# Kernel optimization log

Measured on AMD Instinct MI355X. Metric: run time of the kernel, lower is better.

The kernel has to match this reference:

```python
import jax, jax.numpy as jnp
import numpy as np

B, C, H, W, HEADS = 8, 256, 64, 64, 4
EPS = 1e-5  # torch InstanceNorm2d default eps


def conv1x1(x, w):
    # w: [out_c, in_c]; x: [b, in_c, h, w]
    return jnp.einsum('oc,bchw->bohw', w, x)


def maxpool2(x):
    b, c, h, w = x.shape
    return x.reshape(b, c, h // 2, 2, w // 2, 2).max(axis=(3, 5))


def inorm_affine(x, g, b):
    # InstanceNorm2d(affine=True): normalize per (batch, channel) over H,W
    m = jnp.mean(x, axis=(2, 3), keepdims=True)
    v = jnp.mean((x - m) ** 2, axis=(2, 3), keepdims=True)
    return (x - m) * jax.lax.rsqrt(v + EPS) * g[None, :, None, None] + b[None, :, None, None]


def setup_inputs() -> dict:
    key = jax.random.key(0)
    ks = jax.random.split(key, 12)
    s = 1.0 / np.sqrt(C)  # fan-in style scaling for 1x1 conv weights
    return {
        'x': jax.random.normal(ks[0], (B, C, H, W), jnp.float32),
        'theta_w': jax.random.normal(ks[1], (C, C), jnp.float32) * s,
        'phi_w': jax.random.normal(ks[2], (C, C), jnp.float32) * s,
        'g_w': jax.random.normal(ks[3], (C // 2, C), jnp.float32) * s,
        'o_w': jax.random.normal(ks[4], (C, C // 2), jnp.float32) * np.sqrt(2.0 / C),
        'nt_w': 1.0 + 0.1 * jax.random.normal(ks[5], (C,), jnp.float32),
        'nt_b': 0.1 * jax.random.normal(ks[6], (C,), jnp.float32),
        'np_w': 1.0 + 0.1 * jax.random.normal(ks[7], (C,), jnp.float32),
        'np_b': 0.1 * jax.random.normal(ks[8], (C,), jnp.float32),
        'ng_w': 1.0 + 0.1 * jax.random.normal(ks[9], (C // 2,), jnp.float32),
        'ng_b': 0.1 * jax.random.normal(ks[10], (C // 2,), jnp.float32),
        'gamma': jnp.float32(0.5),
    }


def reference(x, theta_w, phi_w, g_w, o_w, nt_w, nt_b, np_w, np_b, ng_w, ng_b, gamma):
    b, c, h, w = x.shape
    n = h * w            # query length
    m = n // 4           # key/value length after 2x2 maxpool
    theta = inorm_affine(conv1x1(x, theta_w), nt_w, nt_b)
    phi = inorm_affine(maxpool2(conv1x1(x, phi_w)), np_w, np_b)
    g = inorm_affine(maxpool2(conv1x1(x, g_w)), ng_w, ng_b)
    # custom head layout: channel dim split as (C//heads, heads), head dim INNER
    theta_ = theta.reshape(b, c // HEADS, HEADS, n)
    phi_ = phi.reshape(b, c // HEADS, HEADS, m)
    g_ = g.reshape(b, (c // 2) // HEADS, HEADS, m)
    beta = jax.nn.softmax(jnp.einsum('bchi,bchj->bhij', theta_, phi_), axis=-1)
    o = jnp.einsum('bchj,bhij->bchi', g_, beta).reshape(b, c // 2, h, w)
    o = conv1x1(o, o_w)
    return gamma * o + x
```

## Files before the change

### kernel.cpp

```cpp
#include <hip/hip_runtime.h>
#include <hip/hip_bf16.h>
#include <math.h>

typedef float f32x4 __attribute__((ext_vector_type(4)));
typedef float f32x16 __attribute__((ext_vector_type(16)));
typedef __bf16 b16x8 __attribute__((ext_vector_type(8)));
typedef __bf16 b16x4 __attribute__((ext_vector_type(4)));
typedef unsigned int u32x2 __attribute__((ext_vector_type(2)));
typedef unsigned int u32x4 __attribute__((ext_vector_type(4)));

#define L2E 1.44269504088896340736f

__global__ void prep_weights(const float* tw, const float* pw, const float* gw,
                             const float* ow, __bf16* Wp, __bf16* OWp) {
    int idx = blockIdx.x * 256 + threadIdx.x;
    if (idx < 640 * 256) {
        int m = idx >> 8, k = idx & 255;
        float v;
        if (m < 256)      { int o = ((m & 63) << 2) + (m >> 6);            v = tw[o * 256 + k]; }
        else if (m < 512) { int mm = m - 256; int o = ((mm & 63) << 2) + (mm >> 6); v = pw[o * 256 + k]; }
        else              { int mm = m - 512; int o = ((mm & 31) << 2) + (mm >> 5); v = gw[o * 256 + k]; }
        Wp[idx] = (__bf16)v;
    } else {
        int j = idx - 640 * 256;
        if (j < 256 * 128) {
            int m = j >> 7, c = j & 127;
            int o = ((c & 31) << 2) + (c >> 5);
            OWp[j] = (__bf16)ow[m * 128 + o];
        }
    }
}

__global__ void transpose_x(const float* x, __bf16* xt) {
    __shared__ float tile[32][33];
    int b = blockIdx.z, c0 = blockIdx.y * 32, p0 = blockIdx.x * 32;
    int tx = threadIdx.x & 31, ty = threadIdx.x >> 5;
#pragma unroll
    for (int i = 0; i < 4; i++) {
        int cy = ty + i * 8;
        tile[cy][tx] = x[((size_t)(b * 256 + c0 + cy)) * 4096 + p0 + tx];
    }
    __syncthreads();
#pragma unroll
    for (int i = 0; i < 4; i++) {
        int py = ty + i * 8;
        xt[((size_t)b * 4096 + p0 + py) * 256 + c0 + tx] = (__bf16)tile[tx][py];
    }
}

__global__ __launch_bounds__(256) void conv_gemm(const __bf16* __restrict__ Wp,
                                                 const __bf16* __restrict__ xt,
                                                 __bf16* theta_t, __bf16* phi_t, __bf16* g_t) {
    int b = blockIdx.z, mt = blockIdx.y, nt = blockIdx.x;
    __shared__ __bf16 Al[128 * 40];
    __shared__ __bf16 Bl[128 * 40];
    int tid = threadIdx.x, l = tid & 63, w = tid >> 6;
    int wm = w >> 1, wn = w & 1, lr = l & 15, lg = l >> 4;
    f32x4 acc[4][4];
#pragma unroll
    for (int i = 0; i < 4; i++)
#pragma unroll
        for (int j = 0; j < 4; j++)
#pragma unroll
            for (int r = 0; r < 4; r++) acc[i][j][r] = 0.f;
    const __bf16* Ag = Wp + (size_t)mt * 128 * 256;
    const __bf16* Bg = xt + ((size_t)b * 4096 + nt * 128) * 256;
    int srow = tid >> 2, scol = (tid & 3) * 8;
    for (int k0 = 0; k0 < 256; k0 += 32) {
        __syncthreads();
#pragma unroll
        for (int hh = 0; hh < 2; hh++) {
            int r = srow + hh * 64;
            *(b16x8*)&Al[r * 40 + scol] = *(const b16x8*)&Ag[(size_t)r * 256 + k0 + scol];
            *(b16x8*)&Bl[r * 40 + scol] = *(const b16x8*)&Bg[(size_t)r * 256 + k0 + scol];
        }
        __syncthreads();
        int ko = lg * 8;
        b16x8 af[4], bfr[4];
#pragma unroll
        for (int i = 0; i < 4; i++) af[i]  = *(b16x8*)&Al[(wm * 64 + i * 16 + lr) * 40 + ko];
#pragma unroll
        for (int i = 0; i < 4; i++) bfr[i] = *(b16x8*)&Bl[(wn * 64 + i * 16 + lr) * 40 + ko];
#pragma unroll
        for (int i = 0; i < 4; i++)
#pragma unroll
            for (int j = 0; j < 4; j++)
                acc[i][j] = __builtin_amdgcn_mfma_f32_16x16x32_bf16(af[i], bfr[j], acc[i][j], 0, 0, 0);
    }
    int rbase = lg * 4;
#pragma unroll
    for (int i = 0; i < 4; i++) {
        int m = mt * 128 + wm * 64 + i * 16 + rbase;
#pragma unroll
        for (int j = 0; j < 4; j++) {
            int p = nt * 128 + wn * 64 + j * 16 + lr;
            b16x4 v;
#pragma unroll
            for (int r = 0; r < 4; r++) v[r] = (__bf16)acc[i][j][r];
            if (m < 256)      *(b16x4*)&theta_t[((size_t)b * 4096 + p) * 256 + m] = v;
            else if (m < 512) *(b16x4*)&phi_t[((size_t)b * 4096 + p) * 256 + (m - 256)] = v;
            else              *(b16x4*)&g_t[((size_t)b * 4096 + p) * 128 + (m - 512)] = v;
        }
    }
}

__global__ void theta_stats(const __bf16* __restrict__ src, float* p1, float* p2) {
    int b = blockIdx.y, rc = blockIdx.x, c = threadIdx.x;
    float a1 = 0.f, a2 = 0.f;
    for (int r = 0; r < 256; r++) {
        float v = (float)src[((size_t)b * 4096 + rc * 256 + r) * 256 + c];
        a1 += v; a2 += v * v;
    }
    p1[(b * 16 + rc) * 256 + c] = a1;
    p2[(b * 16 + rc) * 256 + c] = a2;
}

__global__ void pool_phi(const __bf16* __restrict__ src, __bf16* dst, float* p1, float* p2) {
    int b = blockIdx.y, qc = blockIdx.x, c = threadIdx.x;
    float a1 = 0.f, a2 = 0.f;
    for (int qq = 0; qq < 32; qq++) {
        int q = qc * 32 + qq, qy = q >> 5, qx = q & 31;
        size_t base = ((size_t)(b * 4096) + qy * 128 + qx * 2) * 256 + c;
        float v0 = (float)src[base], v1 = (float)src[base + 256];
        float v2 = (float)src[base + 16384], v3 = (float)src[base + 16640];
        float m = fmaxf(fmaxf(v0, v1), fmaxf(v2, v3));
        dst[((size_t)b * 1024 + q) * 256 + c] = (__bf16)m;
        a1 += m; a2 += m * m;
    }
    p1[(b * 32 + qc) * 256 + c] = a1;
    p2[(b * 32 + qc) * 256 + c] = a2;
}

__global__ __launch_bounds__(256) void pool_gT(const __bf16* __restrict__ src, __bf16* gT,
                                               float* p1, float* p2) {
    __shared__ __bf16 Pt[64][136];
    int b = blockIdx.y, qc = blockIdx.x;
    int t = threadIdx.x, c = t & 127, qh = t >> 7;
    float a1 = 0.f, a2 = 0.f;
    for (int qq = 0; qq < 32; qq++) {
        int ql = qh * 32 + qq, q = qc * 64 + ql;
        int qy = q >> 5, qx = q & 31;
        size_t base = ((size_t)(b * 4096) + qy * 128 + qx * 2) * 128 + c;
        float v0 = (float)src[base], v1 = (float)src[base + 128];
        float v2 = (float)src[base + 8192], v3 = (float)src[base + 8320];
        float m = fmaxf(fmaxf(v0, v1), fmaxf(v2, v3));
        Pt[ql][c] = (__bf16)m;
        a1 += m; a2 += m * m;
    }
    p1[(b * 16 + qc) * 256 + t] = a1;
    p2[(b * 16 + qc) * 256 + t] = a2;
    __syncthreads();
    int hh = c >> 5, ch = c & 31;
#pragma unroll
    for (int sg = 0; sg < 4; sg++) {
        int seg = qh * 4 + sg;
        b16x8 v;
#pragma unroll
        for (int e = 0; e < 8; e++) v[e] = Pt[seg * 8 + e][c];
        *(b16x8*)&gT[((((size_t)(b * 4 + hh) * 16 + qc) * 8 + seg) * 32 + ch) * 8] = v;
    }
}

__global__ void finalize_stats(const float* tp1, const float* tp2, const float* pp1,
                               const float* pp2, const float* gp1, const float* gp2,
                               const float* ntw, const float* ntb, const float* npw,
                               const float* npb, const float* ngw, const float* ngb,
                               float* sct, float* bit, float* scp, float* bip,
                               float* scg, float* big) {
    int idx = blockIdx.x * 256 + threadIdx.x;
    if (idx >= 8 * 640) return;
    int b = idx / 640, c = idx % 640;
    if (c < 256) {
        float s1 = 0.f, s2 = 0.f;
        for (int i = 0; i < 16; i++) { s1 += tp1[(b * 16 + i) * 256 + c]; s2 += tp2[(b * 16 + i) * 256 + c]; }
        float n = 4096.f;
        float m = s1 / n, v = s2 / n - m * m;
        float r = rsqrtf(v + 1e-5f);
        int o = ((c & 63) << 2) + (c >> 6);
        float wv = ntw[o], bv = ntb[o];
        sct[b * 256 + c] = r * wv * L2E;
        bit[b * 256 + c] = (bv - m * r * wv) * L2E;
    } else if (c < 512) {
        int cc = c - 256;
        float s1 = 0.f, s2 = 0.f;
        for (int i = 0; i < 32; i++) { s1 += pp1[(b * 32 + i) * 256 + cc]; s2 += pp2[(b * 32 + i) * 256 + cc]; }
        float n = 1024.f;
        float m = s1 / n, v = s2 / n - m * m;
        float r = rsqrtf(v + 1e-5f);
        int o = ((cc & 63) << 2) + (cc >> 6);
        float wv = npw[o], bv = npb[o];
        scp[b * 256 + cc] = r * wv; bip[b * 256 + cc] = bv - m * r * wv;
    } else {
        int cc = c - 512;
        float s1 = 0.f, s2 = 0.f;
        for (int i = 0; i < 16; i++) {
            s1 += gp1[(b * 16 + i) * 256 + cc] + gp1[(b * 16 + i) * 256 + 128 + cc];
            s2 += gp2[(b * 16 + i) * 256 + cc] + gp2[(b * 16 + i) * 256 + 128 + cc];
        }
        float n = 1024.f;
        float m = s1 / n, v = s2 / n - m * m;
        float r = rsqrtf(v + 1e-5f);
        int o = ((cc & 31) << 2) + (cc >> 5);
        float wv = ngw[o], bv = ngb[o];
        scg[b * 128 + cc] = r * wv; big[b * 128 + cc] = bv - m * r * wv;
    }
}

__global__ void normalize_phi(const __bf16* __restrict__ php, __bf16* __restrict__ phk,
                              const float* __restrict__ scp, const float* __restrict__ bip) {
    int blk = blockIdx.x, t = threadIdx.x;
    int b = blk >> 6, h = (blk >> 4) & 3, cc = blk & 15;
#pragma unroll
    for (int uu = 0; uu < 2; uu++) {
        int u = uu * 256 + t;
        int slot = u >> 6, key = u & 63;
        int q = cc * 64 + key;
        int cfull = h * 64 + (slot >> 1) * 16 + (slot & 1) * 8;
        b16x8 v = *(const b16x8*)&php[((size_t)b * 1024 + q) * 256 + cfull];
        b16x8 nv;
#pragma unroll
        for (int e = 0; e < 8; e++)
            nv[e] = (__bf16)((float)v[e] * scp[b * 256 + cfull + e] + bip[b * 256 + cfull + e]);
        *(b16x8*)&phk[((((size_t)(b * 4 + h) * 16 + cc) * 8 + slot) * 64 + key) * 8] = nv;
    }
}

__global__ __launch_bounds__(256, 2) void attn(const __bf16* __restrict__ theta_t,
                                               const __bf16* __restrict__ phk,
                                               const __bf16* __restrict__ gTz,
                                               const float* __restrict__ sct,
                                               const float* __restrict__ bit,
                                               const float* __restrict__ scg,
                                               const float* __restrict__ big,
                                               __bf16* __restrict__ o_mid) {
    int bid = blockIdx.x;
    int idx = bid >> 3;
    int bh = (bid & 7) * 4 + (idx >> 4), qt = idx & 15;
    int b = bh >> 2, h = bh & 3;
    int tid = threadIdx.x, w = tid >> 6, lane = tid & 63;
    int l31 = lane & 31, hi = lane >> 5;
    int qb = qt * 256 + w * 64;

    b16x8 qf[2][4];
#pragma unroll
    for (int m = 0; m < 2; m++) {
        int q = qb + m * 32 + l31;
        const __bf16* qp = theta_t + ((size_t)b * 4096 + q) * 256 + h * 64;
#pragma unroll
        for (int st = 0; st < 4; st++) {
            int cb = st * 16 + hi * 8;
            b16x8 raw = *(const b16x8*)&qp[cb];
            b16x8 nv;
#pragma unroll
            for (int e = 0; e < 8; e++) {
                int cix = b * 256 + h * 64 + cb + e;
                nv[e] = (__bf16)((float)raw[e] * sct[cix] + bit[cix]);
            }
            qf[m][st] = nv;
        }
    }

    const __bf16* Kg = phk + (size_t)bh * 65536 + (size_t)hi * 512 + (size_t)l31 * 8;
    const __bf16* Vg = gTz + (size_t)bh * 32768 + (size_t)hi * 256 + (size_t)l31 * 8;

    f32x16 oacc[2];
    float l_run[2] = {0.f, 0.f};
#pragma unroll
    for (int m = 0; m < 2; m++)
#pragma unroll
        for (int r = 0; r < 16; r++) oacc[m][r] = 0.f;
    f32x16 zc;
#pragma unroll
    for (int r = 0; r < 16; r++) zc[r] = 0.f;

    b16x8 akA[2][4], avA[4], akB[2][4], avB[4];

#define LOADK(dst, c) { _Pragma("unroll") for (int kf = 0; kf < 2; kf++) \
    _Pragma("unroll") for (int st = 0; st < 4; st++) \
        dst[kf][st] = *(const b16x8*)&Kg[(size_t)(c) * 4096 + st * 1024 + kf * 256]; }
#define LOADV(dst, c) { _Pragma("unroll") for (int js = 0; js < 4; js++) \
    dst[js] = *(const b16x8*)&Vg[(size_t)(c) * 2048 + js * 512]; }
#define COMPUTE(ak, av) { \
    _Pragma("unroll") for (int m = 0; m < 2; m++) { \
        _Pragma("unroll") for (int kf = 0; kf < 2; kf++) { \
            f32x16 s = __builtin_amdgcn_mfma_f32_32x32x16_bf16(ak[kf][0], qf[m][0], zc, 0, 0, 0); \
            _Pragma("unroll") for (int st = 1; st < 4; st++) \
                s = __builtin_amdgcn_mfma_f32_32x32x16_bf16(ak[kf][st], qf[m][st], s, 0, 0, 0); \
            float sum = 0.f; \
            _Pragma("unroll") for (int r = 0; r < 16; r++) { \
                float p = __builtin_amdgcn_exp2f(s[r]); s[r] = p; sum += p; } \
            l_run[m] += sum; \
            _Pragma("unroll") for (int hh2 = 0; hh2 < 2; hh2++) { \
                b16x4 A4, B4; \
                _Pragma("unroll") for (int e = 0; e < 4; e++) { \
                    A4[e] = (__bf16)s[hh2 * 8 + e]; B4[e] = (__bf16)s[hh2 * 8 + 4 + e]; } \
                u32x2 a2 = __builtin_bit_cast(u32x2, A4); \
                u32x2 b2 = __builtin_bit_cast(u32x2, B4); \
                u32x2 q0 = __builtin_amdgcn_permlane32_swap(a2[0], b2[0], false, false); \
                u32x2 q1 = __builtin_amdgcn_permlane32_swap(a2[1], b2[1], false, false); \
                u32x4 pd = {q0[0], q1[0], q0[1], q1[1]}; \
                b16x8 pf = __builtin_bit_cast(b16x8, pd); \
                oacc[m] = __builtin_amdgcn_mfma_f32_32x32x16_bf16(av[kf * 2 + hh2], pf, oacc[m], 0, 0, 0); \
            } \
        } \
    } }

    LOADK(akA, 0) LOADV(avA, 0)
#pragma unroll 1
    for (int c = 0; c < 16; c += 2) {
        LOADK(akB, c + 1) LOADV(avB, c + 1)
        COMPUTE(akA, avA)
        if (c + 2 < 16) { LOADK(akA, c + 2) LOADV(avA, c + 2) }
        COMPUTE(akB, avB)
    }
#undef LOADK
#undef LOADV
#undef COMPUTE

#pragma unroll
    for (int m = 0; m < 2; m++) {
        float lr = l_run[m] + __shfl_xor(l_run[m], 32, 64);
        float rl = 1.0f / lr;
        int q = qb + m * 32 + l31;
#pragma unroll
        for (int rr = 0; rr < 4; rr++) {
            b16x4 v;
#pragma unroll
            for (int e = 0; e < 4; e++) {
                int ci = b * 128 + h * 32 + rr * 8 + hi * 4 + e;
                v[e] = (__bf16)(oacc[m][rr * 4 + e] * rl * scg[ci] + big[ci]);
            }
            *(b16x4*)&o_mid[((size_t)b * 4096 + q) * 128 + h * 32 + rr * 8 + hi * 4] = v;
        }
    }
}

__global__ __launch_bounds__(256) void out_gemm(const __bf16* __restrict__ OWp,
                                                const __bf16* __restrict__ o_mid,
                                                const float* __restrict__ x,
                                                const float* gamma, float* out) {
    int b = blockIdx.z, mt = blockIdx.y, nt = blockIdx.x;
    __shared__ __bf16 Al[128 * 40];
    __shared__ __bf16 Bl[128 * 40];
    int tid = threadIdx.x, l = tid & 63, w = tid >> 6;
    int wm = w >> 1, wn = w & 1, lr = l & 15, lg = l >> 4;
    f32x4 acc[4][4];
#pragma unroll
    for (int i = 0; i < 4; i++)
#pragma unroll
        for (int j = 0; j < 4; j++)
#pragma unroll
            for (int r = 0; r < 4; r++) acc[i][j][r] = 0.f;
    const __bf16* Ag = OWp + (size_t)mt * 128 * 128;
    const __bf16* Bg = o_mid + ((size_t)b * 4096 + nt * 128) * 128;
    int srow = tid >> 2, scol = (tid & 3) * 8;
    for (int k0 = 0; k0 < 128; k0 += 32) {
        __syncthreads();
#pragma unroll
        for (int hh = 0; hh < 2; hh++) {
            int r = srow + hh * 64;
            *(b16x8*)&Al[r * 40 + scol] = *(const b16x8*)&Ag[(size_t)r * 128 + k0 + scol];
            *(b16x8*)&Bl[r * 40 + scol] = *(const b16x8*)&Bg[(size_t)r * 128 + k0 + scol];
        }
        __syncthreads();
        int ko = lg * 8;
        b16x8 af[4], bfr[4];
#pragma unroll
        for (int i = 0; i < 4; i++) af[i]  = *(b16x8*)&Al[(wm * 64 + i * 16 + lr) * 40 + ko];
#pragma unroll
        for (int i = 0; i < 4; i++) bfr[i] = *(b16x8*)&Bl[(wn * 64 + i * 16 + lr) * 40 + ko];
#pragma unroll
        for (int i = 0; i < 4; i++)
#pragma unroll
            for (int j = 0; j < 4; j++)
                acc[i][j] = __builtin_amdgcn_mfma_f32_16x16x32_bf16(af[i], bfr[j], acc[i][j], 0, 0, 0);
    }
    float gm = gamma[0];
    int rbase = lg * 4;
#pragma unroll
    for (int i = 0; i < 4; i++) {
        int m = mt * 128 + wm * 64 + i * 16 + rbase;
#pragma unroll
        for (int j = 0; j < 4; j++) {
            int p = nt * 128 + wn * 64 + j * 16 + lr;
#pragma unroll
            for (int r = 0; r < 4; r++) {
                size_t o = ((size_t)b * 256 + m + r) * 4096 + p;
                out[o] = gm * acc[i][j][r] + x[o];
            }
        }
    }
}

extern "C" void kernel_launch(void* const* d_in, const int* in_sizes, int n_in,
                              void* d_out, int out_size, void* d_ws, size_t ws_size,
                              hipStream_t stream) {
    const float* x   = (const float*)d_in[0];
    const float* tw  = (const float*)d_in[1];
    const float* pw  = (const float*)d_in[2];
    const float* gw  = (const float*)d_in[3];
    const float* ow  = (const float*)d_in[4];
    const float* ntw = (const float*)d_in[5];
    const float* ntb = (const float*)d_in[6];
    const float* npw = (const float*)d_in[7];
    const float* npb = (const float*)d_in[8];
    const float* ngw = (const float*)d_in[9];
    const float* ngb = (const float*)d_in[10];
    const float* gamma = (const float*)d_in[11];
    float* out = (float*)d_out;
    char* ws = (char*)d_ws;

    __bf16* Wp  = (__bf16*)(ws + 0);
    __bf16* OWp = (__bf16*)(ws + 327680);
    __bf16* xt  = (__bf16*)(ws + 393216);
    __bf16* th  = (__bf16*)(ws + 17170432);
    __bf16* phr = (__bf16*)(ws + 33947648);
    __bf16* ghr = (__bf16*)(ws + 50724864);
    __bf16* php = (__bf16*)(ws + 59113472);
    __bf16* gT  = (__bf16*)(ws + 63307776);
    float* sb   = (float*)(ws + 65445888);

    float* tp1 = (float*)(ws + 393216);
    float* tp2 = (float*)(ws + 524288);
    float* pp1 = (float*)(ws + 655360);
    float* pp2 = (float*)(ws + 917504);
    float* gp1 = (float*)(ws + 1179648);
    float* gp2 = (float*)(ws + 1310720);
    __bf16* phk = phr;
    __bf16* om  = xt;

    float *sct = sb, *bit = sb + 2048, *scp = sb + 4096, *bip = sb + 6144,
          *scg = sb + 8192, *big = sb + 9216;

    prep_weights<<<768, 256, 0, stream>>>(tw, pw, gw, ow, Wp, OWp);
    transpose_x<<<dim3(128, 8, 8), 256, 0, stream>>>(x, xt);
    conv_gemm<<<dim3(32, 5, 8), 256, 0, stream>>>(Wp, xt, th, phr, ghr);
    theta_stats<<<dim3(16, 8), 256, 0, stream>>>(th, tp1, tp2);
    pool_phi<<<dim3(32, 8), 256, 0, stream>>>(phr, php, pp1, pp2);
    pool_gT<<<dim3(16, 8), 256, 0, stream>>>(ghr, gT, gp1, gp2);
    finalize_stats<<<20, 256, 0, stream>>>(tp1, tp2, pp1, pp2, gp1, gp2,
                                           ntw, ntb, npw, npb, ngw, ngb,
                                           sct, bit, scp, bip, scg, big);
    normalize_phi<<<512, 256, 0, stream>>>(php, phk, scp, bip);
    attn<<<512, 256, 0, stream>>>(th, phk, gT, sct, bit, scg, big, om);
    out_gemm<<<dim3(32, 2, 8), 256, 0, stream>>>(OWp, om, x, gamma, out);
}
```

Baseline: 129.5 us.

## Split attention keys across waves, vectorize stats kernels, prefetch GEMM tiles

The attention kernel now gives each block 128 queries and splits the key range between wave pairs, so twice as many blocks launch. Partial outputs and row sums are combined through shared memory, and the kernel adds s_setprio hints and split exp-sum accumulators. The stats and pooling kernels switch from scalar to 8-wide vector loads with a shared-memory reduction. Both GEMMs register-prefetch the next K tile. The aim is better occupancy and memory throughput, at the cost of an extra shared-memory combine and a larger partial-stats buffer.

```diff
diff --git a/kernel.cpp b/kernel.cpp
--- a/kernel.cpp
+++ b/kernel.cpp
@@ -66,15 +66,30 @@
     const __bf16* Ag = Wp + (size_t)mt * 128 * 256;
     const __bf16* Bg = xt + ((size_t)b * 4096 + nt * 128) * 256;
     int srow = tid >> 2, scol = (tid & 3) * 8;
+    b16x8 aR[2], bR[2];
+#pragma unroll
+    for (int hh = 0; hh < 2; hh++) {
+        int r = srow + hh * 64;
+        aR[hh] = *(const b16x8*)&Ag[(size_t)r * 256 + scol];
+        bR[hh] = *(const b16x8*)&Bg[(size_t)r * 256 + scol];
+    }
     for (int k0 = 0; k0 < 256; k0 += 32) {
-        __syncthreads();
+        if (k0) __syncthreads();
 #pragma unroll
         for (int hh = 0; hh < 2; hh++) {
             int r = srow + hh * 64;
-            *(b16x8*)&Al[r * 40 + scol] = *(const b16x8*)&Ag[(size_t)r * 256 + k0 + scol];
-            *(b16x8*)&Bl[r * 40 + scol] = *(const b16x8*)&Bg[(size_t)r * 256 + k0 + scol];
+            *(b16x8*)&Al[r * 40 + scol] = aR[hh];
+            *(b16x8*)&Bl[r * 40 + scol] = bR[hh];
         }
         __syncthreads();
+        if (k0 < 224) {
+#pragma unroll
+            for (int hh = 0; hh < 2; hh++) {
+                int r = srow + hh * 64;
+                aR[hh] = *(const b16x8*)&Ag[(size_t)r * 256 + k0 + 32 + scol];
+                bR[hh] = *(const b16x8*)&Bg[(size_t)r * 256 + k0 + 32 + scol];
+            }
+        }
         int ko = lg * 8;
         b16x8 af[4], bfr[4];
 #pragma unroll
@@ -104,52 +119,102 @@
     }
 }
 
-__global__ void theta_stats(const __bf16* __restrict__ src, float* p1, float* p2) {
-    int b = blockIdx.y, rc = blockIdx.x, c = threadIdx.x;
-    float a1 = 0.f, a2 = 0.f;
-    for (int r = 0; r < 256; r++) {
-        float v = (float)src[((size_t)b * 4096 + rc * 256 + r) * 256 + c];
-        a1 += v; a2 += v * v;
-    }
-    p1[(b * 16 + rc) * 256 + c] = a1;
-    p2[(b * 16 + rc) * 256 + c] = a2;
-}
-
-__global__ void pool_phi(const __bf16* __restrict__ src, __bf16* dst, float* p1, float* p2) {
-    int b = blockIdx.y, qc = blockIdx.x, c = threadIdx.x;
-    float a1 = 0.f, a2 = 0.f;
-    for (int qq = 0; qq < 32; qq++) {
-        int q = qc * 32 + qq, qy = q >> 5, qx = q & 31;
-        size_t base = ((size_t)(b * 4096) + qy * 128 + qx * 2) * 256 + c;
-        float v0 = (float)src[base], v1 = (float)src[base + 256];
-        float v2 = (float)src[base + 16384], v3 = (float)src[base + 16640];
-        float m = fmaxf(fmaxf(v0, v1), fmaxf(v2, v3));
-        dst[((size_t)b * 1024 + q) * 256 + c] = (__bf16)m;
-        a1 += m; a2 += m * m;
-    }
-    p1[(b * 32 + qc) * 256 + c] = a1;
-    p2[(b * 32 + qc) * 256 + c] = a2;
+__global__ __launch_bounds__(256) void theta_stats(const __bf16* __restrict__ src,
+                                                   float* p1, float* p2) {
+    __shared__ float S1[8][256], S2[8][256];
+    int b = blockIdx.y, blk = blockIdx.x;
+    int tid = threadIdx.x, cg = tid & 31, rg = tid >> 5;
+    float a1[8], a2[8];
+#pragma unroll
+    for (int e = 0; e < 8; e++) { a1[e] = 0.f; a2[e] = 0.f; }
+    const __bf16* base = src + ((size_t)b * 4096 + blk * 64 + rg * 8) * 256 + cg * 8;
+#pragma unroll
+    for (int r = 0; r < 8; r++) {
+        b16x8 v = *(const b16x8*)&base[(size_t)r * 256];
+#pragma unroll
+        for (int e = 0; e < 8; e++) { float f = (float)v[e]; a1[e] += f; a2[e] += f * f; }
+    }
+#pragma unroll
+    for (int e = 0; e < 8; e++) { S1[rg][cg * 8 + e] = a1[e]; S2[rg][cg * 8 + e] = a2[e]; }
+    __syncthreads();
+    float s1 = 0.f, s2 = 0.f;
+#pragma unroll
+    for (int i = 0; i < 8; i++) { s1 += S1[i][tid]; s2 += S2[i][tid]; }
+    p1[(b * 64 + blk) * 256 + tid] = s1;
+    p2[(b * 64 + blk) * 256 + tid] = s2;
+}
+
+__global__ __launch_bounds__(256) void pool_phi(const __bf16* __restrict__ src, __bf16* dst,
+                                                float* p1, float* p2) {
+    __shared__ float S1[8][256], S2[8][256];
+    int b = blockIdx.y, qc = blockIdx.x;
+    int tid = threadIdx.x, cg = tid & 31, qg = tid >> 5;
+    float a1[8], a2[8];
+#pragma unroll
+    for (int e = 0; e < 8; e++) { a1[e] = 0.f; a2[e] = 0.f; }
+#pragma unroll
+    for (int qq = 0; qq < 4; qq++) {
+        int q = qc * 32 + qg * 4 + qq, qy = q >> 5, qx = q & 31;
+        size_t base = ((size_t)(b * 4096) + qy * 128 + qx * 2) * 256 + cg * 8;
+        b16x8 v0 = *(const b16x8*)&src[base];
+        b16x8 v1 = *(const b16x8*)&src[base + 256];
+        b16x8 v2 = *(const b16x8*)&src[base + 16384];
+        b16x8 v3 = *(const b16x8*)&src[base + 16640];
+        b16x8 mv;
+#pragma unroll
+        for (int e = 0; e < 8; e++) {
+            float m = fmaxf(fmaxf((float)v0[e], (float)v1[e]), fmaxf((float)v2[e], (float)v3[e]));
+            mv[e] = (__bf16)m; a1[e] += m; a2[e] += m * m;
+        }
+        *(b16x8*)&dst[((size_t)b * 1024 + q) * 256 + cg * 8] = mv;
+    }
+#pragma unroll
+    for (int e = 0; e < 8; e++) { S1[qg][cg * 8 + e] = a1[e]; S2[qg][cg * 8 + e] = a2[e]; }
+    __syncthreads();
+    float s1 = 0.f, s2 = 0.f;
+#pragma unroll
+    for (int i = 0; i < 8; i++) { s1 += S1[i][tid]; s2 += S2[i][tid]; }
+    p1[(b * 32 + qc) * 256 + tid] = s1;
+    p2[(b * 32 + qc) * 256 + tid] = s2;
 }
 
 __global__ __launch_bounds__(256) void pool_gT(const __bf16* __restrict__ src, __bf16* gT,
                                                float* p1, float* p2) {
     __shared__ __bf16 Pt[64][136];
+    __shared__ float S1[16][128], S2[16][128];
     int b = blockIdx.y, qc = blockIdx.x;
-    int t = threadIdx.x, c = t & 127, qh = t >> 7;
-    float a1 = 0.f, a2 = 0.f;
-    for (int qq = 0; qq < 32; qq++) {
-        int ql = qh * 32 + qq, q = qc * 64 + ql;
+    int tid = threadIdx.x, cg = tid & 15, qg = tid >> 4;
+    float a1[8], a2[8];
+#pragma unroll
+    for (int e = 0; e < 8; e++) { a1[e] = 0.f; a2[e] = 0.f; }
+#pragma unroll
+    for (int qq = 0; qq < 4; qq++) {
+        int ql = qg * 4 + qq, q = qc * 64 + ql;
         int qy = q >> 5, qx = q & 31;
-        size_t base = ((size_t)(b * 4096) + qy * 128 + qx * 2) * 128 + c;
-        float v0 = (float)src[base], v1 = (float)src[base + 128];
-        float v2 = (float)src[base + 8192], v3 = (float)src[base + 8320];
-        float m = fmaxf(fmaxf(v0, v1), fmaxf(v2, v3));
-        Pt[ql][c] = (__bf16)m;
-        a1 += m; a2 += m * m;
-    }
-    p1[(b * 16 + qc) * 256 + t] = a1;
-    p2[(b * 16 + qc) * 256 + t] = a2;
+        size_t base = ((size_t)(b * 4096) + qy * 128 + qx * 2) * 128 + cg * 8;
+        b16x8 v0 = *(const b16x8*)&src[base];
+        b16x8 v1 = *(const b16x8*)&src[base + 128];
+        b16x8 v2 = *(const b16x8*)&src[base + 8192];
+        b16x8 v3 = *(const b16x8*)&src[base + 8320];
+        b16x8 mv;
+#pragma unroll
+        for (int e = 0; e < 8; e++) {
+            float m = fmaxf(fmaxf((float)v0[e], (float)v1[e]), fmaxf((float)v2[e], (float)v3[e]));
+            mv[e] = (__bf16)m; a1[e] += m; a2[e] += m * m;
+        }
+        *(b16x8*)&Pt[ql][cg * 8] = mv;
+    }
+#pragma unroll
+    for (int e = 0; e < 8; e++) { S1[qg][cg * 8 + e] = a1[e]; S2[qg][cg * 8 + e] = a2[e]; }
     __syncthreads();
+    if (tid < 128) {
+        float s1 = 0.f, s2 = 0.f;
+#pragma unroll
+        for (int i = 0; i < 16; i++) { s1 += S1[i][tid]; s2 += S2[i][tid]; }
+        p1[(b * 16 + qc) * 128 + tid] = s1;
+        p2[(b * 16 + qc) * 128 + tid] = s2;
+    }
+    int c = tid & 127, qh = tid >> 7;
     int hh = c >> 5, ch = c & 31;
 #pragma unroll
     for (int sg = 0; sg < 4; sg++) {
@@ -172,7 +237,7 @@
     int b = idx / 640, c = idx % 640;
     if (c < 256) {
         float s1 = 0.f, s2 = 0.f;
-        for (int i = 0; i < 16; i++) { s1 += tp1[(b * 16 + i) * 256 + c]; s2 += tp2[(b * 16 + i) * 256 + c]; }
+        for (int i = 0; i < 64; i++) { s1 += tp1[(b * 64 + i) * 256 + c]; s2 += tp2[(b * 64 + i) * 256 + c]; }
         float n = 4096.f;
         float m = s1 / n, v = s2 / n - m * m;
         float r = rsqrtf(v + 1e-5f);
@@ -193,10 +258,7 @@
     } else {
         int cc = c - 512;
         float s1 = 0.f, s2 = 0.f;
-        for (int i = 0; i < 16; i++) {
-            s1 += gp1[(b * 16 + i) * 256 + cc] + gp1[(b * 16 + i) * 256 + 128 + cc];
-            s2 += gp2[(b * 16 + i) * 256 + cc] + gp2[(b * 16 + i) * 256 + 128 + cc];
-        }
+        for (int i = 0; i < 16; i++) { s1 += gp1[(b * 16 + i) * 128 + cc]; s2 += gp2[(b * 16 + i) * 128 + cc]; }
         float n = 1024.f;
         float m = s1 / n, v = s2 / n - m * m;
         float r = rsqrtf(v + 1e-5f);
@@ -225,7 +287,7 @@
     }
 }
 
-__global__ __launch_bounds__(256, 2) void attn(const __bf16* __restrict__ theta_t,
+__global__ __launch_bounds__(256, 4) void attn(const __bf16* __restrict__ theta_t,
                                                const __bf16* __restrict__ phk,
                                                const __bf16* __restrict__ gTz,
                                                const float* __restrict__ sct,
@@ -233,13 +295,15 @@
                                                const float* __restrict__ scg,
                                                const float* __restrict__ big,
                                                __bf16* __restrict__ o_mid) {
+    __shared__ float comb[2][64][34];
     int bid = blockIdx.x;
     int idx = bid >> 3;
-    int bh = (bid & 7) * 4 + (idx >> 4), qt = idx & 15;
+    int bh = (bid & 7) * 4 + (idx >> 5), qt = idx & 31;
     int b = bh >> 2, h = bh & 3;
     int tid = threadIdx.x, w = tid >> 6, lane = tid & 63;
     int l31 = lane & 31, hi = lane >> 5;
-    int qb = qt * 256 + w * 64;
+    int wq = w >> 1, wk = w & 1;
+    int qb = qt * 128 + wq * 64;
 
     b16x8 qf[2][4];
 #pragma unroll
@@ -283,13 +347,21 @@
 #define COMPUTE(ak, av) { \
     _Pragma("unroll") for (int m = 0; m < 2; m++) { \
         _Pragma("unroll") for (int kf = 0; kf < 2; kf++) { \
+            __builtin_amdgcn_s_setprio(1); \
             f32x16 s = __builtin_amdgcn_mfma_f32_32x32x16_bf16(ak[kf][0], qf[m][0], zc, 0, 0, 0); \
             _Pragma("unroll") for (int st = 1; st < 4; st++) \
                 s = __builtin_amdgcn_mfma_f32_32x32x16_bf16(ak[kf][st], qf[m][st], s, 0, 0, 0); \
-            float sum = 0.f; \
-            _Pragma("unroll") for (int r = 0; r < 16; r++) { \
-                float p = __builtin_amdgcn_exp2f(s[r]); s[r] = p; sum += p; } \
-            l_run[m] += sum; \
+            __builtin_amdgcn_s_setprio(0); \
+            float s0 = 0.f, s1 = 0.f, s2p = 0.f, s3 = 0.f; \
+            _Pragma("unroll") for (int r = 0; r < 16; r += 4) { \
+                float p0 = __builtin_amdgcn_exp2f(s[r]); \
+                float p1 = __builtin_amdgcn_exp2f(s[r + 1]); \
+                float p2 = __builtin_amdgcn_exp2f(s[r + 2]); \
+                float p3 = __builtin_amdgcn_exp2f(s[r + 3]); \
+                s[r] = p0; s[r + 1] = p1; s[r + 2] = p2; s[r + 3] = p3; \
+                s0 += p0; s1 += p1; s2p += p2; s3 += p3; \
+            } \
+            l_run[m] += (s0 + s1) + (s2p + s3); \
             _Pragma("unroll") for (int hh2 = 0; hh2 < 2; hh2++) { \
                 b16x4 A4, B4; \
                 _Pragma("unroll") for (int e = 0; e < 4; e++) { \
@@ -300,37 +372,60 @@
                 u32x2 q1 = __builtin_amdgcn_permlane32_swap(a2[1], b2[1], false, false); \
                 u32x4 pd = {q0[0], q1[0], q0[1], q1[1]}; \
                 b16x8 pf = __builtin_bit_cast(b16x8, pd); \
+                __builtin_amdgcn_s_setprio(1); \
                 oacc[m] = __builtin_amdgcn_mfma_f32_32x32x16_bf16(av[kf * 2 + hh2], pf, oacc[m], 0, 0, 0); \
+                __builtin_amdgcn_s_setprio(0); \
             } \
         } \
     } }
 
-    LOADK(akA, 0) LOADV(avA, 0)
+    int c0 = wk * 8;
+    LOADK(akA, c0) LOADV(avA, c0)
 #pragma unroll 1
-    for (int c = 0; c < 16; c += 2) {
+    for (int cc = 0; cc < 8; cc += 2) {
+        int c = c0 + cc;
         LOADK(akB, c + 1) LOADV(avB, c + 1)
         COMPUTE(akA, avA)
-        if (c + 2 < 16) { LOADK(akA, c + 2) LOADV(avA, c + 2) }
+        if (cc + 2 < 8) { LOADK(akA, c + 2) LOADV(avA, c + 2) }
         COMPUTE(akB, avB)
     }
 #undef LOADK
 #undef LOADV
 #undef COMPUTE
 
-#pragma unroll
-    for (int m = 0; m < 2; m++) {
-        float lr = l_run[m] + __shfl_xor(l_run[m], 32, 64);
-        float rl = 1.0f / lr;
-        int q = qb + m * 32 + l31;
-#pragma unroll
-        for (int rr = 0; rr < 4; rr++) {
-            b16x4 v;
-#pragma unroll
-            for (int e = 0; e < 4; e++) {
-                int ci = b * 128 + h * 32 + rr * 8 + hi * 4 + e;
-                v[e] = (__bf16)(oacc[m][rr * 4 + e] * rl * scg[ci] + big[ci]);
+    if (wk == 1) {
+#pragma unroll
+        for (int r = 0; r < 16; r++) {
+            comb[wq][lane][r] = oacc[0][r];
+            comb[wq][lane][16 + r] = oacc[1][r];
+        }
+        comb[wq][lane][32] = l_run[0];
+        comb[wq][lane][33] = l_run[1];
+    }
+    __syncthreads();
+    if (wk == 0) {
+#pragma unroll
+        for (int r = 0; r < 16; r++) {
+            oacc[0][r] += comb[wq][lane][r];
+            oacc[1][r] += comb[wq][lane][16 + r];
+        }
+        l_run[0] += comb[wq][lane][32];
+        l_run[1] += comb[wq][lane][33];
+#pragma unroll
+        for (int m = 0; m < 2; m++) {
+            float lr = l_run[m] + __shfl_xor(l_run[m], 32, 64);
+            float rl = 1.0f / lr;
+            int q = qb + m * 32 + l31;
+#pragma unroll
+            for (int rr = 0; rr < 4; rr++) {
+                b16x4 v;
+#pragma unroll
+                for (int e = 0; e < 4; e++) {
+                    int ci = b * 128 + h * 32 + rr * 8 + hi * 4 + e;
+                    v[e] = (__bf16)(oacc[m][rr * 4 + e] * rl * scg[ci] + big[ci]);
+                }
+                *(b16x4*)&o_mid[((size_t)b * 4096 + q) * 128 + h * 32 + rr * 8 + hi * 4] = v;
             }
-            *(b16x4*)&o_mid[((size_t)b * 4096 + q) * 128 + h * 32 + rr * 8 + hi * 4] = v;
         }
     }
 }
@@ -354,15 +449,30 @@
     const __bf16* Ag = OWp + (size_t)mt * 128 * 128;
     const __bf16* Bg = o_mid + ((size_t)b * 4096 + nt * 128) * 128;
     int srow = tid >> 2, scol = (tid & 3) * 8;
+    b16x8 aR[2], bR[2];
+#pragma unroll
+    for (int hh = 0; hh < 2; hh++) {
+        int r = srow + hh * 64;
+        aR[hh] = *(const b16x8*)&Ag[(size_t)r * 128 + scol];
+        bR[hh] = *(const b16x8*)&Bg[(size_t)r * 128 + scol];
+    }
     for (int k0 = 0; k0 < 128; k0 += 32) {
-        __syncthreads();
+        if (k0) __syncthreads();
 #pragma unroll
         for (int hh = 0; hh < 2; hh++) {
             int r = srow + hh * 64;
-            *(b16x8*)&Al[r * 40 + scol] = *(const b16x8*)&Ag[(size_t)r * 128 + k0 + scol];
-            *(b16x8*)&Bl[r * 40 + scol] = *(const b16x8*)&Bg[(size_t)r * 128 + k0 + scol];
+            *(b16x8*)&Al[r * 40 + scol] = aR[hh];
+            *(b16x8*)&Bl[r * 40 + scol] = bR[hh];
         }
         __syncthreads();
+        if (k0 < 96) {
+#pragma unroll
+            for (int hh = 0; hh < 2; hh++) {
+                int r = srow + hh * 64;
+                aR[hh] = *(const b16x8*)&Ag[(size_t)r * 128 + k0 + 32 + scol];
+                bR[hh] = *(const b16x8*)&Bg[(size_t)r * 128 + k0 + 32 + scol];
+            }
+        }
         int ko = lg * 8;
         b16x8 af[4], bfr[4];
 #pragma unroll
@@ -421,11 +531,11 @@
     float* sb   = (float*)(ws + 65445888);
 
     float* tp1 = (float*)(ws + 393216);
-    float* tp2 = (float*)(ws + 524288);
-    float* pp1 = (float*)(ws + 655360);
-    float* pp2 = (float*)(ws + 917504);
-    float* gp1 = (float*)(ws + 1179648);
-    float* gp2 = (float*)(ws + 1310720);
+    float* tp2 = (float*)(ws + 917504);
+    float* pp1 = (float*)(ws + 1441792);
+    float* pp2 = (float*)(ws + 1703936);
+    float* gp1 = (float*)(ws + 1966080);
+    float* gp2 = (float*)(ws + 2031616);
     __bf16* phk = phr;
     __bf16* om  = xt;
 
@@ -435,13 +545,13 @@
     prep_weights<<<768, 256, 0, stream>>>(tw, pw, gw, ow, Wp, OWp);
     transpose_x<<<dim3(128, 8, 8), 256, 0, stream>>>(x, xt);
     conv_gemm<<<dim3(32, 5, 8), 256, 0, stream>>>(Wp, xt, th, phr, ghr);
-    theta_stats<<<dim3(16, 8), 256, 0, stream>>>(th, tp1, tp2);
+    theta_stats<<<dim3(64, 8), 256, 0, stream>>>(th, tp1, tp2);
     pool_phi<<<dim3(32, 8), 256, 0, stream>>>(phr, php, pp1, pp2);
     pool_gT<<<dim3(16, 8), 256, 0, stream>>>(ghr, gT, gp1, gp2);
     finalize_stats<<<20, 256, 0, stream>>>(tp1, tp2, pp1, pp2, gp1, gp2,
                                            ntw, ntb, npw, npb, ngw, ngb,
                                            sct, bit, scp, bip, scg, big);
     normalize_phi<<<512, 256, 0, stream>>>(php, phk, scp, bip);
-    attn<<<512, 256, 0, stream>>>(th, phk, gT, sct, bit, scg, big, om);
+    attn<<<1024, 256, 0, stream>>>(th, phk, gT, sct, bit, scg, big, om);
     out_gemm<<<dim3(32, 2, 8), 256, 0, stream>>>(OWp, om, x, gamma, out);
 }
```

Result: slower. 474.9 us (+266.7%).
